# Optimization experiments

Hardware: AMD Instinct MI355X
Metric: run time of the kernel (lower is better)

The kernel has to match this reference:

```python
import jax, jax.numpy as jnp
import numpy as np

TAU = 0.5

def setup_inputs() -> dict:
    key = jax.random.key(0)
    kx, ky = jax.random.split(key)
    B, H = 8192, 256
    x = jax.random.normal(kx, (B, H), dtype=jnp.float32)
    y = jax.random.normal(ky, (B, H), dtype=jnp.float32)
    return {"x": x, "y": y}

def reference(x, y):
    # L2-normalize rows
    x_norm = x / jnp.linalg.norm(x, axis=1, keepdims=True)
    y_norm = y / jnp.linalg.norm(y, axis=1, keepdims=True)
    xy_norm = jnp.concatenate([x_norm, y_norm], axis=0)  # [2N, H]
    yx_norm = jnp.concatenate([y_norm, x_norm], axis=0)  # [2N, H]
    # [2N, 2N] cosine-similarity matrix (dominant memory traffic)
    sim_mat_1 = xy_norm @ xy_norm.T
    exp_mat = jnp.exp(sim_mat_1 / TAU)
    exp_row_sum = jnp.sum(exp_mat, axis=1)
    exp_diag = jnp.diagonal(exp_mat)
    denominator = exp_row_sum - exp_diag
    # diag(xy_norm @ yx_norm.T) is the row-wise dot product (avoids redundant NxN matmul)
    pos_sim = jnp.sum(xy_norm * yx_norm, axis=1)
    numerator = jnp.exp(pos_sim / TAU)
    nt_xent = -jnp.log(numerator / denominator)
    return jnp.mean(nt_xent)
```

## Files before the change

kernel.cpp:

```cpp
#include <hip/hip_runtime.h>
#include <hip/hip_bf16.h>
#include <math.h>

constexpr int NROWS = 8192;
constexpr int HDIM  = 256;
constexpr int N2    = 16384;
constexpr int BM    = 128;
constexpr int BK    = 32;
constexpr int NCHUNK = HDIM / BK;
constexpr int NTILE = N2 / BM;
constexpr int NBLK  = NTILE * (NTILE + 1) / 2;

constexpr float PRESCALE = 1.69864357f;

typedef __attribute__((ext_vector_type(4))) float floatx4;
typedef __attribute__((ext_vector_type(8))) short shortx8;

__device__ __forceinline__ void async_copy16(const void* gptr, void* lptr) {
    __builtin_amdgcn_global_load_lds(
        (const __attribute__((address_space(1))) unsigned int*)gptr,
        (__attribute__((address_space(3))) unsigned int*)lptr, 16, 0, 0);
}

#define WAIT_VM4()   __builtin_amdgcn_s_waitcnt(0x0F74)
#define WAIT_VM0()   __builtin_amdgcn_s_waitcnt(0x0F70)
#define MEMFENCE()   __asm__ __volatile__("" ::: "memory")
#define RAW_BARRIER() do { MEMFENCE(); __builtin_amdgcn_s_barrier(); MEMFENCE(); } while (0)

#define DPP_ROW_SHL_ADD(v, CTRL) do {                                        \
    union { float f; int i; } _u, _r; _u.f = (v);                            \
    _r.i = __builtin_amdgcn_update_dpp(0, _u.i, (CTRL), 0xF, 0xF, true);     \
    (v) += _r.f; } while (0)

__global__ __launch_bounds__(256) void normalize_kernel(
    const float* __restrict__ x, const float* __restrict__ y,
    __hip_bfloat16* __restrict__ Z, float* __restrict__ pos,
    float* __restrict__ rowsum, float* __restrict__ out)
{
    const int wave = threadIdx.x >> 6, lane = threadIdx.x & 63;
    const int row  = blockIdx.x * 4 + wave;

    const float4 xv = ((const float4*)x)[row * 64 + lane];
    const float4 yv = ((const float4*)y)[row * 64 + lane];

    float sx  = xv.x*xv.x + xv.y*xv.y + xv.z*xv.z + xv.w*xv.w;
    float sy  = yv.x*yv.x + yv.y*yv.y + yv.z*yv.z + yv.w*yv.w;
    float sxy = xv.x*yv.x + xv.y*yv.y + xv.z*yv.z + xv.w*yv.w;
    #pragma unroll
    for (int m = 1; m < 64; m <<= 1) {
        sx  += __shfl_xor(sx,  m);
        sy  += __shfl_xor(sy,  m);
        sxy += __shfl_xor(sxy, m);
    }
    const float rxn = rsqrtf(sx), ryn = rsqrtf(sy);
    const float rx = rxn * PRESCALE, ry = ryn * PRESCALE;

    union { ushort4 u; __hip_bfloat16 h[4]; } zx, zy;
    zx.h[0] = __float2bfloat16(xv.x * rx); zx.h[1] = __float2bfloat16(xv.y * rx);
    zx.h[2] = __float2bfloat16(xv.z * rx); zx.h[3] = __float2bfloat16(xv.w * rx);
    zy.h[0] = __float2bfloat16(yv.x * ry); zy.h[1] = __float2bfloat16(yv.y * ry);
    zy.h[2] = __float2bfloat16(yv.z * ry); zy.h[3] = __float2bfloat16(yv.w * ry);
    ((ushort4*)Z)[row * 64 + lane]             = zx.u;
    ((ushort4*)Z)[(row + NROWS) * 64 + lane]   = zy.u;

    if (lane == 0) {
        const float p = sxy * rxn * ryn;
        pos[row]         = p;
        pos[row + NROWS] = p;
    }
    const int gt = blockIdx.x * 256 + threadIdx.x;
    if (gt < N2) rowsum[gt] = 0.f;
    if (gt == 0) out[0] = 0.f;
}

__global__ __launch_bounds__(256, 3) void simgemm_kernel(
    const __hip_bfloat16* __restrict__ Z, float* __restrict__ rowsum)
{
    const int b = blockIdx.x;
    const int k = b & 7;
    const int m = b >> 3;
    int bi, bj;
    if (m < 136) {
        int ti = (int)((33.0f - sqrtf(1089.0f - 8.0f * (float)m)) * 0.5f);
        if (m < ti * (33 - ti) / 2) ti--;
        else if (m >= (ti + 1) * (32 - ti) / 2) ti++;
        const int tj = ti + (m - ti * (33 - ti) / 2);
        bi = k * 16 + ti;
        bj = k * 16 + tj;
    } else {
        const int m2 = m - 136;
        const int hh = m2 >> 7;
        const int r  = m2 & 127;
        const int h  = hh * 8 + k;
        const int q  = h >> 1;
        const int sub = h & 1;
        int gi = 0;
        #pragma unroll
        for (int t = 6; t > 0; --t)
            if (q >= t * (15 - t) / 2) { gi = t; break; }
        const int gj = gi + 1 + (q - gi * (15 - gi) / 2);
        bi = gi * 16 + sub * 8 + (r >> 4);
        bj = gj * 16 + (r & 15);
    }
    const bool diag = (bi == bj);

    __shared__ alignas(16) __hip_bfloat16 tiles[6 * BM * BK];
    __shared__ float rs[BM];
    __shared__ float cs[BM];
    __hip_bfloat16* tA = tiles;
    __hip_bfloat16* tB = tiles + BM * BK;

    const int tid  = threadIdx.x;
    const int wave = tid >> 6;
    const int lane = tid & 63;
    const int wm   = wave & 1;
    const int wn   = wave >> 1;
    const int g    = lane >> 4;
    const int m15  = lane & 15;

    if (tid < BM) { rs[tid] = 0.f; cs[tid] = 0.f; }

    const int st_r0  = wave * 32 + (lane >> 2);
    const int st_c   = (lane & 3) ^ ((lane >> 3) & 3);
    const __hip_bfloat16* gA0 = Z + (size_t)(bi * BM + st_r0) * HDIM + st_c * 8;
    const __hip_bfloat16* gA1 = gA0 + 16 * HDIM;
    const __hip_bfloat16* gB0 = Z + (size_t)(bj * BM + st_r0) * HDIM + st_c * 8;
    const __hip_bfloat16* gB1 = gB0 + 16 * HDIM;
    __hip_bfloat16* lA0 = tA + (wave * 32) * BK;
    __hip_bfloat16* lA1 = tA + (wave * 32 + 16) * BK;
    __hip_bfloat16* lB0 = tB + (wave * 32) * BK;
    __hip_bfloat16* lB1 = tB + (wave * 32 + 16) * BK;

    const int sw = g ^ ((m15 >> 1) & 3);
    const __hip_bfloat16* rA = tA + (wm * 64 + m15) * BK + sw * 8;
    const __hip_bfloat16* rB = tB + (wn * 64 + m15) * BK + sw * 8;

    floatx4 acc[4][4] = {};

    #define STAGE(ck)  do {                                                  \
        const int _o = ((ck) % 3) * 2 * BM * BK;                             \
        async_copy16(gA0 + (ck) * BK, lA0 + _o);                             \
        async_copy16(gA1 + (ck) * BK, lA1 + _o);                             \
        async_copy16(gB0 + (ck) * BK, lB0 + _o);                             \
        async_copy16(gB1 + (ck) * BK, lB1 + _o);                             \
    } while (0)

    STAGE(0);

    #pragma unroll
    for (int s = 0; s < NCHUNK; ++s) {
        if (s + 1 < NCHUNK) { STAGE(s + 1); WAIT_VM4(); }
        else                { WAIT_VM0(); }
        RAW_BARRIER();

        const int bo = (s % 3) * 2 * BM * BK;
        shortx8 af[4], bfr[4];
        #pragma unroll
        for (int f = 0; f < 4; ++f) {
            af[f]  = *(const shortx8*)(rA + bo + f * 16 * BK);
            bfr[f] = *(const shortx8*)(rB + bo + f * 16 * BK);
        }
        #pragma unroll
        for (int fm = 0; fm < 4; ++fm)
            #pragma unroll
            for (int fn = 0; fn < 4; ++fn)
                acc[fm][fn] = __builtin_amdgcn_mfma_f32_16x16x32_bf16(
                    af[fm], bfr[fn], acc[fm][fn], 0, 0, 0);
    }
    #undef STAGE

    float rp[4][4] = {{0.f}};
    float cp[4]    = {0.f};

    if (!diag) {
        #pragma unroll
        for (int fm = 0; fm < 4; ++fm)
            #pragma unroll
            for (int fn = 0; fn < 4; ++fn) {
                const floatx4 a = acc[fm][fn];
                #pragma unroll
                for (int q = 0; q < 4; ++q) {
                    const float e = __builtin_amdgcn_exp2f(a[q]);
                    rp[fm][q] += e;
                    cp[fn]    += e;
                }
            }
    } else {
        #pragma unroll
        for (int fm = 0; fm < 4; ++fm)
            #pragma unroll
            for (int fn = 0; fn < 4; ++fn) {
                const floatx4 a = acc[fm][fn];
                const int cl = wn * 64 + fn * 16 + m15;
                #pragma unroll
                for (int q = 0; q < 4; ++q) {
                    const int rl = wm * 64 + fm * 16 + g * 4 + q;
                    float e = __builtin_amdgcn_exp2f(a[q]);
                    if (cl <= rl) e = 0.f;
                    rp[fm][q] += e;
                    cp[fn]    += e;
                }
            }
    }

    #pragma unroll
    for (int fm = 0; fm < 4; ++fm)
        #pragma unroll
        for (int q = 0; q < 4; ++q) {
            float v = rp[fm][q];
            DPP_ROW_SHL_ADD(v, 0x101);
            DPP_ROW_SHL_ADD(v, 0x102);
            DPP_ROW_SHL_ADD(v, 0x104);
            DPP_ROW_SHL_ADD(v, 0x108);
            rp[fm][q] = v;
        }
    if (m15 == 0) {
        #pragma unroll
        for (int fm = 0; fm < 4; ++fm)
            #pragma unroll
            for (int q = 0; q < 4; ++q)
                atomicAdd(&rs[wm * 64 + fm * 16 + g * 4 + q], rp[fm][q]);
    }

    #pragma unroll
    for (int mask = 16; mask < 64; mask <<= 1)
        #pragma unroll
        for (int fn = 0; fn < 4; ++fn)
            cp[fn] += __shfl_xor(cp[fn], mask);
    if (g == 0) {
        #pragma unroll
        for (int fn = 0; fn < 4; ++fn)
            atomicAdd(&cs[wn * 64 + fn * 16 + m15], cp[fn]);
    }

    __syncthreads();
    if (tid < BM) {
        atomicAdd(&rowsum[(size_t)bi * BM + tid], rs[tid]);
        atomicAdd(&rowsum[(size_t)bj * BM + tid], cs[tid]);
    }
}

__global__ __launch_bounds__(1024) void finalize_kernel(
    const float* __restrict__ rowsum, const float* __restrict__ pos,
    float* __restrict__ out)
{
    const int i = threadIdx.x + blockIdx.x * 1024;
    float s = logf(rowsum[i]) - 2.0f * pos[i];
    #pragma unroll
    for (int off = 32; off; off >>= 1) s += __shfl_down(s, off);
    __shared__ float sh[16];
    const int lt = threadIdx.x;
    if ((lt & 63) == 0) sh[lt >> 6] = s;
    __syncthreads();
    if (lt == 0) {
        float tot = 0.f;
        #pragma unroll
        for (int w = 0; w < 16; ++w) tot += sh[w];
        atomicAdd(out, tot / (float)N2);
    }
}

extern "C" void kernel_launch(void* const* d_in, const int* in_sizes, int n_in,
                              void* d_out, int out_size, void* d_ws, size_t ws_size,
                              hipStream_t stream)
{
    const float* x = (const float*)d_in[0];
    const float* y = (const float*)d_in[1];

    __hip_bfloat16* Z = (__hip_bfloat16*)d_ws;
    float* rowsum = (float*)((char*)d_ws + (size_t)N2 * HDIM * sizeof(__hip_bfloat16));
    float* pos    = rowsum + N2;

    normalize_kernel<<<NROWS / 4, 256, 0, stream>>>(x, y, Z, pos, rowsum, (float*)d_out);
    simgemm_kernel<<<NBLK, 256, 0, stream>>>(Z, rowsum);
    finalize_kernel<<<N2 / 1024, 1024, 0, stream>>>(rowsum, pos, (float*)d_out);
}
```

Baseline: 157.3 us.

## Pre-pack Z in MFMA fragment order and load operands directly from global

The normalize kernel now writes the bf16 normalized rows in a packed layout matching the MFMA 16x16x32 operand fragment order. That lets the GEMM kernel load each wave's A/B fragments straight from global/L2 into registers, with register double-buffering. This removes the LDS staging, async global-to-LDS copies, waitcnts and per-chunk barriers. In exchange each wave fetches its fragments separately instead of sharing them through LDS, so global/L2 traffic rises and global load latency is exposed more directly.

```diff
diff --git a/kernel.cpp b/kernel.cpp
--- a/kernel.cpp
+++ b/kernel.cpp
@@ -6,8 +6,6 @@
 constexpr int HDIM  = 256;
 constexpr int N2    = 16384;
 constexpr int BM    = 128;
-constexpr int BK    = 32;
-constexpr int NCHUNK = HDIM / BK;
 constexpr int NTILE = N2 / BM;
 constexpr int NBLK  = NTILE * (NTILE + 1) / 2;
 
@@ -15,26 +13,16 @@
 
 typedef __attribute__((ext_vector_type(4))) float floatx4;
 typedef __attribute__((ext_vector_type(8))) short shortx8;
-
-__device__ __forceinline__ void async_copy16(const void* gptr, void* lptr) {
-    __builtin_amdgcn_global_load_lds(
-        (const __attribute__((address_space(1))) unsigned int*)gptr,
-        (__attribute__((address_space(3))) unsigned int*)lptr, 16, 0, 0);
-}
-
-#define WAIT_VM4()   __builtin_amdgcn_s_waitcnt(0x0F74)
-#define WAIT_VM0()   __builtin_amdgcn_s_waitcnt(0x0F70)
-#define MEMFENCE()   __asm__ __volatile__("" ::: "memory")
-#define RAW_BARRIER() do { MEMFENCE(); __builtin_amdgcn_s_barrier(); MEMFENCE(); } while (0)
 
 #define DPP_ROW_SHL_ADD(v, CTRL) do {                                        \
     union { float f; int i; } _u, _r; _u.f = (v);                            \
     _r.i = __builtin_amdgcn_update_dpp(0, _u.i, (CTRL), 0xF, 0xF, true);     \
     (v) += _r.f; } while (0)
 
+
 __global__ __launch_bounds__(256) void normalize_kernel(
     const float* __restrict__ x, const float* __restrict__ y,
-    __hip_bfloat16* __restrict__ Z, float* __restrict__ pos,
+    __hip_bfloat16* __restrict__ Zp, float* __restrict__ pos,
     float* __restrict__ rowsum, float* __restrict__ out)
 {
     const int wave = threadIdx.x >> 6, lane = threadIdx.x & 63;
@@ -60,8 +48,11 @@
     zx.h[2] = __float2bfloat16(xv.z * rx); zx.h[3] = __float2bfloat16(xv.w * rx);
     zy.h[0] = __float2bfloat16(yv.x * ry); zy.h[1] = __float2bfloat16(yv.y * ry);
     zy.h[2] = __float2bfloat16(yv.z * ry); zy.h[3] = __float2bfloat16(yv.w * ry);
-    ((ushort4*)Z)[row * 64 + lane]             = zx.u;
-    ((ushort4*)Z)[(row + NROWS) * 64 + lane]   = zy.u;
+
+    const int tile = row >> 4, m = row & 15;
+    const size_t off = (size_t)tile * 4096 + (lane >> 1) * 128 + m * 8 + (lane & 1) * 4;
+    *(ushort4*)(Zp + off)                 = zx.u;
+    *(ushort4*)(Zp + off + 512 * 4096)    = zy.u;
 
     if (lane == 0) {
         const float p = sxy * rxn * ryn;
@@ -74,7 +65,7 @@
 }
 
 __global__ __launch_bounds__(256, 3) void simgemm_kernel(
-    const __hip_bfloat16* __restrict__ Z, float* __restrict__ rowsum)
+    const __hip_bfloat16* __restrict__ Zp, float* __restrict__ rowsum)
 {
     const int b = blockIdx.x;
     const int k = b & 7;
@@ -104,11 +95,8 @@
     }
     const bool diag = (bi == bj);
 
-    __shared__ alignas(16) __hip_bfloat16 tiles[6 * BM * BK];
     __shared__ float rs[BM];
     __shared__ float cs[BM];
-    __hip_bfloat16* tA = tiles;
-    __hip_bfloat16* tB = tiles + BM * BK;
 
     const int tid  = threadIdx.x;
     const int wave = tid >> 6;
@@ -119,55 +107,37 @@
     const int m15  = lane & 15;
 
     if (tid < BM) { rs[tid] = 0.f; cs[tid] = 0.f; }
-
-    const int st_r0  = wave * 32 + (lane >> 2);
-    const int st_c   = (lane & 3) ^ ((lane >> 3) & 3);
-    const __hip_bfloat16* gA0 = Z + (size_t)(bi * BM + st_r0) * HDIM + st_c * 8;
-    const __hip_bfloat16* gA1 = gA0 + 16 * HDIM;
-    const __hip_bfloat16* gB0 = Z + (size_t)(bj * BM + st_r0) * HDIM + st_c * 8;
-    const __hip_bfloat16* gB1 = gB0 + 16 * HDIM;
-    __hip_bfloat16* lA0 = tA + (wave * 32) * BK;
-    __hip_bfloat16* lA1 = tA + (wave * 32 + 16) * BK;
-    __hip_bfloat16* lB0 = tB + (wave * 32) * BK;
-    __hip_bfloat16* lB1 = tB + (wave * 32 + 16) * BK;
-
-    const int sw = g ^ ((m15 >> 1) & 3);
-    const __hip_bfloat16* rA = tA + (wm * 64 + m15) * BK + sw * 8;
-    const __hip_bfloat16* rB = tB + (wn * 64 + m15) * BK + sw * 8;
+    __syncthreads();
+
+    const __hip_bfloat16* pA = Zp + (size_t)(bi * 8 + wm * 4) * 4096 + lane * 8;
+    const __hip_bfloat16* pB = Zp + (size_t)(bj * 8 + wn * 4) * 4096 + lane * 8;
 
     floatx4 acc[4][4] = {};
-
-    #define STAGE(ck)  do {                                                  \
-        const int _o = ((ck) % 3) * 2 * BM * BK;                             \
-        async_copy16(gA0 + (ck) * BK, lA0 + _o);                             \
-        async_copy16(gA1 + (ck) * BK, lA1 + _o);                             \
-        async_copy16(gB0 + (ck) * BK, lB0 + _o);                             \
-        async_copy16(gB1 + (ck) * BK, lB1 + _o);                             \
-    } while (0)
-
-    STAGE(0);
-
-    #pragma unroll
-    for (int s = 0; s < NCHUNK; ++s) {
-        if (s + 1 < NCHUNK) { STAGE(s + 1); WAIT_VM4(); }
-        else                { WAIT_VM0(); }
-        RAW_BARRIER();
-
-        const int bo = (s % 3) * 2 * BM * BK;
-        shortx8 af[4], bfr[4];
-        #pragma unroll
-        for (int f = 0; f < 4; ++f) {
-            af[f]  = *(const shortx8*)(rA + bo + f * 16 * BK);
-            bfr[f] = *(const shortx8*)(rB + bo + f * 16 * BK);
+    shortx8 af[2][4], bf[2][4];
+
+    #pragma unroll
+    for (int f = 0; f < 4; ++f) {
+        af[0][f] = *(const shortx8*)(pA + f * 4096);
+        bf[0][f] = *(const shortx8*)(pB + f * 4096);
+    }
+
+    #pragma unroll
+    for (int s = 0; s < HDIM / 32; ++s) {
+        const int cur = s & 1;
+        if (s + 1 < HDIM / 32) {
+            #pragma unroll
+            for (int f = 0; f < 4; ++f) {
+                af[cur ^ 1][f] = *(const shortx8*)(pA + f * 4096 + (s + 1) * 512);
+                bf[cur ^ 1][f] = *(const shortx8*)(pB + f * 4096 + (s + 1) * 512);
+            }
         }
         #pragma unroll
         for (int fm = 0; fm < 4; ++fm)
             #pragma unroll
             for (int fn = 0; fn < 4; ++fn)
                 acc[fm][fn] = __builtin_amdgcn_mfma_f32_16x16x32_bf16(
-                    af[fm], bfr[fn], acc[fm][fn], 0, 0, 0);
-    }
-    #undef STAGE
+                    af[cur][fm], bf[cur][fn], acc[fm][fn], 0, 0, 0);
+    }
 
     float rp[4][4] = {{0.f}};
     float cp[4]    = {0.f};
@@ -267,11 +237,11 @@
     const float* x = (const float*)d_in[0];
     const float* y = (const float*)d_in[1];
 
-    __hip_bfloat16* Z = (__hip_bfloat16*)d_ws;
+    __hip_bfloat16* Zp = (__hip_bfloat16*)d_ws;
     float* rowsum = (float*)((char*)d_ws + (size_t)N2 * HDIM * sizeof(__hip_bfloat16));
     float* pos    = rowsum + N2;
 
-    normalize_kernel<<<NROWS / 4, 256, 0, stream>>>(x, y, Z, pos, rowsum, (float*)d_out);
-    simgemm_kernel<<<NBLK, 256, 0, stream>>>(Z, rowsum);
+    normalize_kernel<<<NROWS / 4, 256, 0, stream>>>(x, y, Zp, pos, rowsum, (float*)d_out);
+    simgemm_kernel<<<NBLK, 256, 0, stream>>>(Zp, rowsum);
     finalize_kernel<<<N2 / 1024, 1024, 0, stream>>>(rowsum, pos, (float*)d_out);
 }
```

Result: slower. 171.5 us (+9.0%).
